# Kernel optimization log

Hardware: AMD Instinct MI355X
Metric: run time of the kernel (lower is better)

## Reference

```python
import jax, jax.numpy as jnp
import numpy as np


def setup_inputs() -> dict:
    key = jax.random.key(0)
    ks = jax.random.split(key, 7)
    B, L, S, H, E, M = 4, 2048, 2048, 8, 64, 4
    return {
        "queries": jax.random.normal(ks[0], (B, L, H, E), dtype=jnp.float32),
        "keys": jax.random.normal(ks[1], (B, S, H, E), dtype=jnp.float32),
        "values": jax.random.normal(ks[2], (B, S, H, E), dtype=jnp.float32),
        "query_omegas": jax.random.normal(ks[3], (B, L, H, M), dtype=jnp.float32),
        "query_thetas": jax.random.normal(ks[4], (B, L, H, M), dtype=jnp.float32),
        "key_omegas": jax.random.normal(ks[5], (B, S, H, M), dtype=jnp.float32),
        "key_thetas": jax.random.normal(ks[6], (B, S, H, M), dtype=jnp.float32),
    }


def _rotate(x, cos, sin, signs):
    # x: (B,T,H,E) split into 4 quaternion components of size E/4
    # cos/sin: (B,T,H,M); output: (B,T,H,M,E) matching torch.cat of einsum pairs
    x0, x1, x2, x3 = jnp.split(x, 4, axis=-1)  # each (B,T,H,E/4)
    c = cos[..., None]  # (B,T,H,M,1)
    s = sin[..., None]
    (a0, b0), (a1, b1), (a2, b2), (a3, b3) = signs
    parts = [
        x0[:, :, :, None, :] * c + a0 * b0[0][:, :, :, None, :] * s if False else None
    ]
    # explicit faithful construction below
    return None


def reference(queries, keys, values, query_omegas, query_thetas, key_omegas, key_thetas):
    B, L, H, E = queries.shape
    S = keys.shape[1]
    M = query_omegas.shape[-1]

    q_pos = (jnp.arange(L, dtype=queries.dtype) / L).reshape(L, 1, 1)
    k_pos = (jnp.arange(S, dtype=keys.dtype) / S).reshape(S, 1, 1)

    Qa = query_omegas * q_pos + query_thetas  # (B,L,H,M)
    Ka = key_omegas * k_pos + key_thetas      # (B,S,H,M)
    Qc, Qs = jnp.cos(Qa)[..., None], jnp.sin(Qa)[..., None]  # (B,L,H,M,1)
    Kc, Ks = jnp.cos(Ka)[..., None], jnp.sin(Ka)[..., None]  # (B,S,H,M,1)

    q0, q1, q2, q3 = [q[:, :, :, None, :] for q in jnp.split(queries, 4, axis=-1)]  # (B,L,H,1,E/4)
    k0, k1, k2, k3 = [k[:, :, :, None, :] for k in jnp.split(keys, 4, axis=-1)]     # (B,S,H,1,E/4)

    Q_rot = jnp.concatenate([
        q0 * Qc - q1 * Qs,
        q1 * Qc + q0 * Qs,
        q2 * Qc + q3 * Qs,
        q3 * Qc - q2 * Qs,
    ], axis=-1)  # (B,L,H,M,E)
    K_rot = jnp.concatenate([
        k0 * Kc - k2 * Ks,
        k1 * Kc - k3 * Ks,
        k2 * Kc + k0 * Ks,
        k3 * Kc + k1 * Ks,
    ], axis=-1)  # (B,S,H,M,E)

    scale = 1.0 / np.sqrt(E)
    scores = jnp.einsum('blhme,bshme->bhls', Q_rot, K_rot) / M  # (B,H,L,S)
    A = jax.nn.softmax(scale * scores, axis=-1)
    V = jnp.einsum('bhls,bshd->blhd', A, values)  # (B,L,H,E)
    return V
```

## Files before the change

### kernel.cpp

```cpp
#include <hip/hip_runtime.h>
#include <math.h>


#define B_ 4
#define L_ 2048
#define S_ 2048
#define H_ 8
#define E_ 64
#define M_ 4
#define QBLK 256
#define NTH 512
#define NTILES 32

#define KROT_OFF 0
#define VTS_OFF  65536
#define PSS_OFF  81920
#define SMEM_BYTES 114688

typedef _Float16 f16x4 __attribute__((ext_vector_type(4)));
typedef _Float16 f16x8 __attribute__((ext_vector_type(8)));
typedef __fp16 fp16x2 __attribute__((ext_vector_type(2)));
typedef float f32x4 __attribute__((ext_vector_type(4)));

union H4U { f16x4 h; fp16x2 p[2]; };
union H8U { f16x8 h; fp16x2 p[4]; };
union F4U { float4 v; float f[4]; };

#if __has_builtin(__builtin_amdgcn_sinf) && __has_builtin(__builtin_amdgcn_cosf)
#define FSINCOS(ang, s, c) do { float _rv = (ang) * 0.15915494309189535f; \
    (s) = __builtin_amdgcn_sinf(_rv); (c) = __builtin_amdgcn_cosf(_rv); } while (0)
#else
#define FSINCOS(ang, s, c) __sincosf((ang), &(s), &(c))
#endif

__device__ __forceinline__ f16x4 cvt4(float x, float y, float z, float w) {
    H4U r;
    r.p[0] = __builtin_amdgcn_cvt_pkrtz(x, y);
    r.p[1] = __builtin_amdgcn_cvt_pkrtz(z, w);
    return r.h;
}
__device__ __forceinline__ f16x8 cvt8(const float* v) {
    H8U r;
#pragma unroll
    for (int i = 0; i < 4; ++i) r.p[i] = __builtin_amdgcn_cvt_pkrtz(v[2 * i], v[2 * i + 1]);
    return r.h;
}

__global__ __launch_bounds__(NTH)
void qattn8(const float* __restrict__ qp, const float* __restrict__ kp,
            const float* __restrict__ vp,
            const float* __restrict__ qo, const float* __restrict__ qt,
            const float* __restrict__ ko, const float* __restrict__ ktt,
            float* __restrict__ out)
{
    const int bid0 = blockIdx.x;
    const int nl = (bid0 & 7) * 32 + (bid0 >> 3);
    const int l0 = (nl & 7) * QBLK;
    const int h  = (nl >> 3) & 7;
    const int b  = nl >> 6;
    const int t  = threadIdx.x;
    const int wv   = t >> 6;
    const int lane = t & 63;
    const int quad = lane >> 4;
    const int nn   = lane & 15;

    __shared__ __align__(16) unsigned char smem[SMEM_BYTES];
    _Float16 (*pss)[64] = reinterpret_cast<_Float16 (*)[64]>(smem + PSS_OFF);
    float (*qstage)[64] = reinterpret_cast<float (*)[64]>(smem);
    float (*qtrc)[4] = reinterpret_cast<float (*)[4]>(smem + PSS_OFF);
    float (*qtrs)[4] = reinterpret_cast<float (*)[4]>(smem + PSS_OFF + 4096);

    const float* kb0 = kp  + ((size_t)((b * S_) * H_ + h)) * E_;
    const float* vb0 = vp  + ((size_t)((b * S_) * H_ + h)) * E_;
    const float* kob = ko  + ((size_t)((b * S_) * H_ + h)) * M_;
    const float* ktb = ktt + ((size_t)((b * S_) * H_ + h)) * M_;

    const int key_r = t >> 3;
    const int ccr   = (t >> 1) & 3;
    const int eh    = t & 1;
    const int swz   = key_r & 7;
    const int tt = t & 255;
    const int kg = tt >> 4;
    const int eg = tt & 15;

    F4U kA[2], kB[2], omR, thR, vv[4];
    auto LOAD = [&](int s0) {
        const float* kr = kb0 + (size_t)(s0 + key_r) * (H_ * E_);
        kA[0].v = *(const float4*)(kr + ccr * 16 + eh * 8);
        kA[1].v = *(const float4*)(kr + ccr * 16 + eh * 8 + 4);
        kB[0].v = *(const float4*)(kr + (ccr ^ 2) * 16 + eh * 8);
        kB[1].v = *(const float4*)(kr + (ccr ^ 2) * 16 + eh * 8 + 4);
        omR.v = *(const float4*)(kob + (size_t)(s0 + key_r) * (H_ * M_));
        thR.v = *(const float4*)(ktb + (size_t)(s0 + key_r) * (H_ * M_));
        if (t >= 256) {
#pragma unroll
            for (int j = 0; j < 4; ++j)
                vv[j].v = *(const float4*)(vb0 + (size_t)(s0 + kg * 4 + j) * (H_ * E_) + eg * 4);
        }
    };

    auto BUILD = [&](int s0, int koff, int voff) {
        _Float16 (*krw)[256] = reinterpret_cast<_Float16 (*)[256]>(smem + koff);
        _Float16 (*vtw)[64]  = reinterpret_cast<_Float16 (*)[64]>(smem + voff);
        {
            float af[8], bf[8];
#pragma unroll
            for (int i2 = 0; i2 < 4; ++i2) {
                af[i2]     = kA[0].f[i2];
                af[4 + i2] = kA[1].f[i2];
                bf[i2]     = kB[0].f[i2];
                bf[4 + i2] = kB[1].f[i2];
            }
            float posk = (float)(s0 + key_r) * (1.0f / S_);
            float kcv[4], ksv[4];
#pragma unroll
            for (int m = 0; m < 4; ++m) {
                float ang = fmaf(omR.f[m], posk, thR.f[m]);
                FSINCOS(ang, ksv[m], kcv[m]);
            }
            const float sgn = (ccr >= 2) ? 1.f : -1.f;
#pragma unroll
            for (int m = 0; m < 4; ++m) {
                float cm = kcv[m], sm = ksv[m] * sgn;
                float vals[8];
#pragma unroll
                for (int i = 0; i < 8; ++i)
                    vals[i] = fmaf(bf[i], sm, af[i] * cm);
                int ch = (m * 8) | ((ccr * 2 + eh) ^ swz);
                *(f16x8*)&krw[key_r][ch * 8] = cvt8(vals);
            }
        }
        if (t >= 256) {
#pragma unroll
            for (int e = 0; e < 4; ++e) {
                int row = eg * 4 + e;
                int ch = ((kg >> 1) ^ (row & 7));
                *(f16x4*)&vtw[row][ch * 8 + (kg & 1) * 4] =
                    cvt4(vv[0].f[e], vv[1].f[e], vv[2].f[e], vv[3].f[e]);
            }
        }
    };

    LOAD(0);

    f16x8 qa[2][8];
    {
        const float* qb = qp + ((size_t)((b * L_ + l0) * H_ + h)) * E_;
#pragma unroll
        for (int i = 0; i < 8; ++i) {
            int idx = t + NTH * i;
            int row = idx >> 4, c16 = idx & 15;
            *(float4*)&qstage[row][c16 * 4] =
                *(const float4*)(qb + (size_t)row * (H_ * E_) + c16 * 4);
        }
        {
            int row = t >> 1, m0 = (t & 1) * 2;
#pragma unroll
            for (int dm = 0; dm < 2; ++dm) {
                int m = m0 + dm;
                size_t off = (size_t)((b * L_ + l0 + row) * H_ + h) * M_ + m;
                float ang = qo[off] * ((float)(l0 + row) * (1.0f / L_)) + qt[off];
                float sv, cv;
                FSINCOS(ang, sv, cv);
                qtrc[row][m] = cv;
                qtrs[row][m] = sv;
            }
        }
        __syncthreads();
#pragma unroll
        for (int set = 0; set < 2; ++set) {
            const int row = wv * 32 + set * 16 + nn;
            const int i0 = (quad & 1) * 8;
            float sl0[8], sl1[8], sl2[8], sl3[8];
            *(float4*)&sl0[0] = *(float4*)&qstage[row][ 0 + i0];
            *(float4*)&sl0[4] = *(float4*)&qstage[row][ 4 + i0];
            *(float4*)&sl1[0] = *(float4*)&qstage[row][16 + i0];
            *(float4*)&sl1[4] = *(float4*)&qstage[row][20 + i0];
            *(float4*)&sl2[0] = *(float4*)&qstage[row][32 + i0];
            *(float4*)&sl2[4] = *(float4*)&qstage[row][36 + i0];
            *(float4*)&sl3[0] = *(float4*)&qstage[row][48 + i0];
            *(float4*)&sl3[4] = *(float4*)&qstage[row][52 + i0];
            const bool hiC = (quad & 2) != 0;
            float aE[8], bE[8], aO[8], bO[8];
#pragma unroll
            for (int j = 0; j < 8; ++j) {
                aE[j] = hiC ? sl1[j] : sl0[j];
                bE[j] = hiC ? sl0[j] : sl1[j];
                aO[j] = hiC ? sl3[j] : sl2[j];
                bO[j] = hiC ? sl2[j] : sl3[j];
            }
            F4U qc4, qs4;
            qc4.v = *(float4*)&qtrc[row][0];
            qs4.v = *(float4*)&qtrs[row][0];
            const float SC = 0.04508422017f;
#pragma unroll
            for (int m = 0; m < 4; ++m) {
                float cm = qc4.f[m] * SC;
                float sm = qs4.f[m] * SC;
                float sE = hiC ? sm : -sm;
                float vE[8], vO[8];
#pragma unroll
                for (int j = 0; j < 8; ++j) {
                    vE[j] = fmaf(bE[j], sE, aE[j] * cm);
                    vO[j] = fmaf(bO[j], -sE, aO[j] * cm);
                }
                qa[set][2 * m]     = cvt8(vE);
                qa[set][2 * m + 1] = cvt8(vO);
            }
        }
        __syncthreads();
    }

    f32x4 Oacc[2][4] = {{{0,0,0,0},{0,0,0,0},{0,0,0,0},{0,0,0,0}},
                        {{0,0,0,0},{0,0,0,0},{0,0,0,0},{0,0,0,0}}};
    float mrow[2] = {-1e30f, -1e30f};
    float lrow[2] = {0.f, 0.f};
    const int xr0 = nn & 7;
    const int swq = (nn & 7) ^ (nn >> 3);

    BUILD(0, KROT_OFF, VTS_OFF);
    LOAD(64);
    __syncthreads();

    for (int ti = 0; ti < NTILES; ++ti) {
        _Float16 (*krot)[256] = reinterpret_cast<_Float16 (*)[256]>(
            smem + KROT_OFF + (ti & 1) * 32768);
        _Float16 (*vts)[64] = reinterpret_cast<_Float16 (*)[64]>(
            smem + VTS_OFF + (ti & 1) * 8192);

        float sc[2][4][4];
        __builtin_amdgcn_s_setprio(1);
#pragma unroll
        for (int kt2 = 0; kt2 < 4; ++kt2) {
            const int keyb = kt2 * 16 + nn;
            f32x4 acc0 = {0, 0, 0, 0}, acc1 = {0, 0, 0, 0};
#pragma unroll
            for (int ks = 0; ks < 8; ++ks) {
                f16x8 bK = *(const f16x8*)&krot[keyb][((ks * 4 + quad) ^ xr0) * 8];
                acc0 = __builtin_amdgcn_mfma_f32_16x16x32_f16(bK, qa[0][ks], acc0, 0, 0, 0);
                acc1 = __builtin_amdgcn_mfma_f32_16x16x32_f16(bK, qa[1][ks], acc1, 0, 0, 0);
            }
#pragma unroll
            for (int r = 0; r < 4; ++r) { sc[0][kt2][r] = acc0[r]; sc[1][kt2][r] = acc1[r]; }
        }
        __builtin_amdgcn_s_setprio(0);

        if (ti + 1 < NTILES) {
            BUILD((ti + 1) * 64, KROT_OFF + ((ti + 1) & 1) * 32768,
                  VTS_OFF + ((ti + 1) & 1) * 8192);
            if (ti + 2 < NTILES) LOAD((ti + 2) * 64);
        }

#pragma unroll
        for (int set = 0; set < 2; ++set) {
            const int rowq = wv * 32 + set * 16 + nn;
            float m01 = fmaxf(fmaxf(sc[set][0][0], sc[set][0][1]), fmaxf(sc[set][0][2], sc[set][0][3]));
            float m23 = fmaxf(fmaxf(sc[set][1][0], sc[set][1][1]), fmaxf(sc[set][1][2], sc[set][1][3]));
            float m45 = fmaxf(fmaxf(sc[set][2][0], sc[set][2][1]), fmaxf(sc[set][2][2], sc[set][2][3]));
            float m67 = fmaxf(fmaxf(sc[set][3][0], sc[set][3][1]), fmaxf(sc[set][3][2], sc[set][3][3]));
            float tm = fmaxf(fmaxf(m01, m23), fmaxf(m45, m67));
            tm = fmaxf(tm, __shfl_xor(tm, 16));
            tm = fmaxf(tm, __shfl_xor(tm, 32));

            if (__any(tm > mrow[set] + 8.0f)) {
                float mnew  = fmaxf(mrow[set], tm);
                float alpha = __builtin_amdgcn_exp2f(mrow[set] - mnew);
                mrow[set] = mnew;
                lrow[set] *= alpha;
#pragma unroll
                for (int r = 0; r < 4; ++r) {
                    float ar = __shfl(alpha, quad * 4 + r, 64);
                    Oacc[set][0][r] *= ar; Oacc[set][1][r] *= ar;
                    Oacc[set][2][r] *= ar; Oacc[set][3][r] *= ar;
                }
            }

            float p[4][4];
#pragma unroll
            for (int kt2 = 0; kt2 < 4; ++kt2)
#pragma unroll
                for (int r = 0; r < 4; ++r)
                    p[kt2][r] = __builtin_amdgcn_exp2f(sc[set][kt2][r] - mrow[set]);

            float s0s = (p[0][0] + p[0][1]) + (p[0][2] + p[0][3]);
            float s1s = (p[1][0] + p[1][1]) + (p[1][2] + p[1][3]);
            float s2s = (p[2][0] + p[2][1]) + (p[2][2] + p[2][3]);
            float s3s = (p[3][0] + p[3][1]) + (p[3][2] + p[3][3]);
            float psum = (s0s + s1s) + (s2s + s3s);
            psum += __shfl_xor(psum, 16);
            psum += __shfl_xor(psum, 32);
            lrow[set] += psum;

#pragma unroll
            for (int kt2 = 0; kt2 < 4; ++kt2) {
                H4U pk;
                pk.p[0] = __builtin_amdgcn_cvt_pkrtz(p[kt2][0], p[kt2][1]);
                pk.p[1] = __builtin_amdgcn_cvt_pkrtz(p[kt2][2], p[kt2][3]);
                int key0 = kt2 * 16 + quad * 4;
                int ch = (key0 >> 3) ^ swq;
                *(f16x4*)&pss[rowq][ch * 8 + (key0 & 7)] = pk.h;
            }
        }

        {
            const int pr0 = wv * 32 + nn;
            __builtin_amdgcn_s_setprio(1);
#pragma unroll
            for (int ks2 = 0; ks2 < 2; ++ks2) {
                f16x8 pf0 = *(const f16x8*)&pss[pr0     ][((quad + 4 * ks2) ^ swq) * 8];
                f16x8 pf1 = *(const f16x8*)&pss[pr0 + 16][((quad + 4 * ks2) ^ swq) * 8];
#pragma unroll
                for (int et = 0; et < 4; ++et) {
                    int e = et * 16 + nn;
                    f16x8 vf = *(const f16x8*)&vts[e][((quad + 4 * ks2) ^ (e & 7)) * 8];
                    Oacc[0][et] = __builtin_amdgcn_mfma_f32_16x16x32_f16(pf0, vf, Oacc[0][et], 0, 0, 0);
                    Oacc[1][et] = __builtin_amdgcn_mfma_f32_16x16x32_f16(pf1, vf, Oacc[1][et], 0, 0, 0);
                }
            }
            __builtin_amdgcn_s_setprio(0);
        }
        __syncthreads();
    }

    float* ob = out + ((size_t)((b * L_ + l0) * H_ + h)) * E_;
#pragma unroll
    for (int set = 0; set < 2; ++set)
#pragma unroll
        for (int r = 0; r < 4; ++r) {
            float lr = __shfl(lrow[set], quad * 4 + r, 64);
            float inv = 1.0f / lr;
            int row = wv * 32 + set * 16 + quad * 4 + r;
#pragma unroll
            for (int et = 0; et < 4; ++et)
                ob[(size_t)row * (H_ * E_) + et * 16 + nn] = Oacc[set][et][r] * inv;
        }
}

extern "C" void kernel_launch(void* const* d_in, const int* in_sizes, int n_in,
                              void* d_out, int out_size, void* d_ws, size_t ws_size,
                              hipStream_t stream) {
    const float* qp = (const float*)d_in[0];
    const float* kp = (const float*)d_in[1];
    const float* vp = (const float*)d_in[2];
    const float* qo = (const float*)d_in[3];
    const float* qt = (const float*)d_in[4];
    const float* ko = (const float*)d_in[5];
    const float* kt = (const float*)d_in[6];
    float* out = (float*)d_out;

    qattn8<<<dim3(B_ * H_ * (L_ / QBLK)), dim3(NTH), 0, stream>>>(
        qp, kp, vp, qo, qt, ko, kt, out);
}
```

Measured before the change: 193.0 us.

## Keep softmax probabilities in registers by permuting key rows in QK MFMA

Reorders which key rows each lane computes in the QK^T MFMA so the score accumulator layout directly matches the A-operand layout of the PV MFMA. The P matrix no longer round-trips through shared memory, which removes the pss buffer, its writes and reads, and shrinks LDS usage from 112KB to 80KB, possibly allowing more resident blocks. The V-transpose and Q staging swizzles are adjusted to avoid bank conflicts under the new access pattern. The risk is that the permuted key row mapping or the new swizzle mismatches between writer and reader.

```diff
diff --git a/kernel.cpp b/kernel.cpp
--- a/kernel.cpp
+++ b/kernel.cpp
@@ -14,8 +14,9 @@
 
 #define KROT_OFF 0
 #define VTS_OFF  65536
-#define PSS_OFF  81920
-#define SMEM_BYTES 114688
+#define QTRC_OFF 73728
+#define QTRS_OFF 77824
+#define SMEM_BYTES 81920
 
 typedef _Float16 f16x4 __attribute__((ext_vector_type(4)));
 typedef _Float16 f16x8 __attribute__((ext_vector_type(8)));
@@ -47,7 +48,7 @@
 }
 
 __global__ __launch_bounds__(NTH)
-void qattn8(const float* __restrict__ qp, const float* __restrict__ kp,
+void qattn9(const float* __restrict__ qp, const float* __restrict__ kp,
             const float* __restrict__ vp,
             const float* __restrict__ qo, const float* __restrict__ qt,
             const float* __restrict__ ko, const float* __restrict__ ktt,
@@ -65,10 +66,9 @@
     const int nn   = lane & 15;
 
     __shared__ __align__(16) unsigned char smem[SMEM_BYTES];
-    _Float16 (*pss)[64] = reinterpret_cast<_Float16 (*)[64]>(smem + PSS_OFF);
-    float (*qstage)[64] = reinterpret_cast<float (*)[64]>(smem);
-    float (*qtrc)[4] = reinterpret_cast<float (*)[4]>(smem + PSS_OFF);
-    float (*qtrs)[4] = reinterpret_cast<float (*)[4]>(smem + PSS_OFF + 4096);
+    float (*qstage)[68] = reinterpret_cast<float (*)[68]>(smem);
+    float (*qtrc)[4] = reinterpret_cast<float (*)[4]>(smem + QTRC_OFF);
+    float (*qtrs)[4] = reinterpret_cast<float (*)[4]>(smem + QTRS_OFF);
 
     const float* kb0 = kp  + ((size_t)((b * S_) * H_ + h)) * E_;
     const float* vb0 = vp  + ((size_t)((b * S_) * H_ + h)) * E_;
@@ -134,7 +134,8 @@
 #pragma unroll
             for (int e = 0; e < 4; ++e) {
                 int row = eg * 4 + e;
-                int ch = ((kg >> 1) ^ (row & 7));
+                int srow = ((row & 7) ^ (row >> 3)) & 7;
+                int ch = (kg >> 1) ^ srow;
                 *(f16x4*)&vtw[row][ch * 8 + (kg & 1) * 4] =
                     cvt4(vv[0].f[e], vv[1].f[e], vv[2].f[e], vv[3].f[e]);
             }
@@ -215,8 +216,8 @@
                         {{0,0,0,0},{0,0,0,0},{0,0,0,0},{0,0,0,0}}};
     float mrow[2] = {-1e30f, -1e30f};
     float lrow[2] = {0.f, 0.f};
-    const int xr0 = nn & 7;
-    const int swq = (nn & 7) ^ (nn >> 3);
+
+    const int sigrow = ((nn >> 2) << 3) + (nn & 3);
 
     BUILD(0, KROT_OFF, VTS_OFF);
     LOAD(64);
@@ -228,21 +229,27 @@
         _Float16 (*vts)[64] = reinterpret_cast<_Float16 (*)[64]>(
             smem + VTS_OFF + (ti & 1) * 8192);
 
-        float sc[2][4][4];
+        float sc[2][2][2][4];
         __builtin_amdgcn_s_setprio(1);
 #pragma unroll
-        for (int kt2 = 0; kt2 < 4; ++kt2) {
-            const int keyb = kt2 * 16 + nn;
-            f32x4 acc0 = {0, 0, 0, 0}, acc1 = {0, 0, 0, 0};
-#pragma unroll
-            for (int ks = 0; ks < 8; ++ks) {
-                f16x8 bK = *(const f16x8*)&krot[keyb][((ks * 4 + quad) ^ xr0) * 8];
-                acc0 = __builtin_amdgcn_mfma_f32_16x16x32_f16(bK, qa[0][ks], acc0, 0, 0, 0);
-                acc1 = __builtin_amdgcn_mfma_f32_16x16x32_f16(bK, qa[1][ks], acc1, 0, 0, 0);
-            }
-#pragma unroll
-            for (int r = 0; r < 4; ++r) { sc[0][kt2][r] = acc0[r]; sc[1][kt2][r] = acc1[r]; }
-        }
+        for (int ks2 = 0; ks2 < 2; ++ks2)
+#pragma unroll
+            for (int hf = 0; hf < 2; ++hf) {
+                const int keyb = ks2 * 32 + hf * 4 + sigrow;
+                const int xr = hf * 4 + (nn & 3);
+                f32x4 acc0 = {0, 0, 0, 0}, acc1 = {0, 0, 0, 0};
+#pragma unroll
+                for (int ks = 0; ks < 8; ++ks) {
+                    f16x8 bK = *(const f16x8*)&krot[keyb][((ks * 4 + quad) ^ xr) * 8];
+                    acc0 = __builtin_amdgcn_mfma_f32_16x16x32_f16(bK, qa[0][ks], acc0, 0, 0, 0);
+                    acc1 = __builtin_amdgcn_mfma_f32_16x16x32_f16(bK, qa[1][ks], acc1, 0, 0, 0);
+                }
+#pragma unroll
+                for (int r = 0; r < 4; ++r) {
+                    sc[0][ks2][hf][r] = acc0[r];
+                    sc[1][ks2][hf][r] = acc1[r];
+                }
+            }
         __builtin_amdgcn_s_setprio(0);
 
         if (ti + 1 < NTILES) {
@@ -251,14 +258,18 @@
             if (ti + 2 < NTILES) LOAD((ti + 2) * 64);
         }
 
+        f16x8 pf[2][2];
 #pragma unroll
         for (int set = 0; set < 2; ++set) {
-            const int rowq = wv * 32 + set * 16 + nn;
-            float m01 = fmaxf(fmaxf(sc[set][0][0], sc[set][0][1]), fmaxf(sc[set][0][2], sc[set][0][3]));
-            float m23 = fmaxf(fmaxf(sc[set][1][0], sc[set][1][1]), fmaxf(sc[set][1][2], sc[set][1][3]));
-            float m45 = fmaxf(fmaxf(sc[set][2][0], sc[set][2][1]), fmaxf(sc[set][2][2], sc[set][2][3]));
-            float m67 = fmaxf(fmaxf(sc[set][3][0], sc[set][3][1]), fmaxf(sc[set][3][2], sc[set][3][3]));
-            float tm = fmaxf(fmaxf(m01, m23), fmaxf(m45, m67));
+            float m0 = fmaxf(fmaxf(sc[set][0][0][0], sc[set][0][0][1]),
+                             fmaxf(sc[set][0][0][2], sc[set][0][0][3]));
+            float m1 = fmaxf(fmaxf(sc[set][0][1][0], sc[set][0][1][1]),
+                             fmaxf(sc[set][0][1][2], sc[set][0][1][3]));
+            float m2 = fmaxf(fmaxf(sc[set][1][0][0], sc[set][1][0][1]),
+                             fmaxf(sc[set][1][0][2], sc[set][1][0][3]));
+            float m3 = fmaxf(fmaxf(sc[set][1][1][0], sc[set][1][1][1]),
+                             fmaxf(sc[set][1][1][2], sc[set][1][1][3]));
+            float tm = fmaxf(fmaxf(m0, m1), fmaxf(m2, m3));
             tm = fmaxf(tm, __shfl_xor(tm, 16));
             tm = fmaxf(tm, __shfl_xor(tm, 32));
 
@@ -275,50 +286,48 @@
                 }
             }
 
-            float p[4][4];
-#pragma unroll
-            for (int kt2 = 0; kt2 < 4; ++kt2)
-#pragma unroll
-                for (int r = 0; r < 4; ++r)
-                    p[kt2][r] = __builtin_amdgcn_exp2f(sc[set][kt2][r] - mrow[set]);
-
-            float s0s = (p[0][0] + p[0][1]) + (p[0][2] + p[0][3]);
-            float s1s = (p[1][0] + p[1][1]) + (p[1][2] + p[1][3]);
-            float s2s = (p[2][0] + p[2][1]) + (p[2][2] + p[2][3]);
-            float s3s = (p[3][0] + p[3][1]) + (p[3][2] + p[3][3]);
+            float p[2][2][4];
+#pragma unroll
+            for (int ks2 = 0; ks2 < 2; ++ks2)
+#pragma unroll
+                for (int hf = 0; hf < 2; ++hf)
+#pragma unroll
+                    for (int r = 0; r < 4; ++r)
+                        p[ks2][hf][r] =
+                            __builtin_amdgcn_exp2f(sc[set][ks2][hf][r] - mrow[set]);
+
+            float s0s = (p[0][0][0] + p[0][0][1]) + (p[0][0][2] + p[0][0][3]);
+            float s1s = (p[0][1][0] + p[0][1][1]) + (p[0][1][2] + p[0][1][3]);
+            float s2s = (p[1][0][0] + p[1][0][1]) + (p[1][0][2] + p[1][0][3]);
+            float s3s = (p[1][1][0] + p[1][1][1]) + (p[1][1][2] + p[1][1][3]);
             float psum = (s0s + s1s) + (s2s + s3s);
             psum += __shfl_xor(psum, 16);
             psum += __shfl_xor(psum, 32);
             lrow[set] += psum;
 
 #pragma unroll
-            for (int kt2 = 0; kt2 < 4; ++kt2) {
-                H4U pk;
-                pk.p[0] = __builtin_amdgcn_cvt_pkrtz(p[kt2][0], p[kt2][1]);
-                pk.p[1] = __builtin_amdgcn_cvt_pkrtz(p[kt2][2], p[kt2][3]);
-                int key0 = kt2 * 16 + quad * 4;
-                int ch = (key0 >> 3) ^ swq;
-                *(f16x4*)&pss[rowq][ch * 8 + (key0 & 7)] = pk.h;
-            }
-        }
-
-        {
-            const int pr0 = wv * 32 + nn;
-            __builtin_amdgcn_s_setprio(1);
-#pragma unroll
             for (int ks2 = 0; ks2 < 2; ++ks2) {
-                f16x8 pf0 = *(const f16x8*)&pss[pr0     ][((quad + 4 * ks2) ^ swq) * 8];
-                f16x8 pf1 = *(const f16x8*)&pss[pr0 + 16][((quad + 4 * ks2) ^ swq) * 8];
-#pragma unroll
-                for (int et = 0; et < 4; ++et) {
-                    int e = et * 16 + nn;
-                    f16x8 vf = *(const f16x8*)&vts[e][((quad + 4 * ks2) ^ (e & 7)) * 8];
-                    Oacc[0][et] = __builtin_amdgcn_mfma_f32_16x16x32_f16(pf0, vf, Oacc[0][et], 0, 0, 0);
-                    Oacc[1][et] = __builtin_amdgcn_mfma_f32_16x16x32_f16(pf1, vf, Oacc[1][et], 0, 0, 0);
-                }
-            }
-            __builtin_amdgcn_s_setprio(0);
-        }
+                H8U pk;
+                pk.p[0] = __builtin_amdgcn_cvt_pkrtz(p[ks2][0][0], p[ks2][0][1]);
+                pk.p[1] = __builtin_amdgcn_cvt_pkrtz(p[ks2][0][2], p[ks2][0][3]);
+                pk.p[2] = __builtin_amdgcn_cvt_pkrtz(p[ks2][1][0], p[ks2][1][1]);
+                pk.p[3] = __builtin_amdgcn_cvt_pkrtz(p[ks2][1][2], p[ks2][1][3]);
+                pf[set][ks2] = pk.h;
+            }
+        }
+
+        __builtin_amdgcn_s_setprio(1);
+#pragma unroll
+        for (int ks2 = 0; ks2 < 2; ++ks2)
+#pragma unroll
+            for (int et = 0; et < 4; ++et) {
+                int e = et * 16 + nn;
+                int se = ((nn & 7) ^ ((et * 2 + (nn >> 3)) & 7)) & 7;
+                f16x8 vf = *(const f16x8*)&vts[e][((quad + 4 * ks2) ^ se) * 8];
+                Oacc[0][et] = __builtin_amdgcn_mfma_f32_16x16x32_f16(pf[0][ks2], vf, Oacc[0][et], 0, 0, 0);
+                Oacc[1][et] = __builtin_amdgcn_mfma_f32_16x16x32_f16(pf[1][ks2], vf, Oacc[1][et], 0, 0, 0);
+            }
+        __builtin_amdgcn_s_setprio(0);
         __syncthreads();
     }
 
@@ -348,6 +357,6 @@
     const float* kt = (const float*)d_in[6];
     float* out = (float*)d_out;
 
-    qattn8<<<dim3(B_ * H_ * (L_ / QBLK)), dim3(NTH), 0, stream>>>(
+    qattn9<<<dim3(B_ * H_ * (L_ / QBLK)), dim3(NTH), 0, stream>>>(
         qp, kp, vp, qo, qt, ko, kt, out);
 }
```

Result: slower. 206.7 us (+7.1%).
